# Kernel tuning notes

Measured on AMD Instinct MI355X. Metric: run time of the kernel, lower is better.

## Reference

```python
import jax, jax.numpy as jnp
import numpy as np

B, H, W, D, K = 64, 32, 32, 64, 512


def setup_inputs() -> dict:
    key = jax.random.key(0)
    k1, k2 = jax.random.split(key)
    x = jax.random.normal(k1, (B, H, W, D), dtype=jnp.float32)
    # tf.random_uniform_initializer default: U(-0.05, 0.05)
    embeddings = jax.random.uniform(k2, (D, K), dtype=jnp.float32,
                                    minval=-0.05, maxval=0.05)
    return {"x": x, "embeddings": embeddings}


def reference(x, embeddings):
    # embeddings: [D, K] (columns are codebook vectors)
    d = embeddings.shape[0]
    flat = x.reshape(-1, d)  # [N, D]
    # squared L2 distance to each code: ||z||^2 + ||e||^2 - 2 z.e
    distances = (jnp.sum(flat * flat, axis=1, keepdims=True)
                 + jnp.sum(embeddings * embeddings, axis=0)
                 - 2.0 * flat @ embeddings)  # [N, K]
    encoding_indices = jnp.argmin(distances, axis=1)  # [N]
    # one-hot @ embeddings^T  ==  gather of codebook rows
    quantized = jnp.take(embeddings.T, encoding_indices, axis=0).reshape(x.shape)
    sg = jax.lax.stop_gradient
    commitment_loss = jnp.mean((sg(quantized) - x) ** 2)  # commitment_cost = 1
    codebook_loss = jnp.mean((quantized - sg(x)) ** 2)
    loss = commitment_loss + codebook_loss
    out = x + sg(quantized - x)  # straight-through estimator
    return out, loss
```

## Files before the change

### kernel.cpp

```cpp
#include <hip/hip_runtime.h>

#define NVEC 65536
#define DIM 64
#define KCODES 512
#define VPB 128
#define NBLK 512
#define NTILE 32
#define ELS 2048.0f
#define GAP_THR 2e-4f

typedef _Float16 f16x8 __attribute__((ext_vector_type(8)));
typedef float    f32x4 __attribute__((ext_vector_type(4)));
typedef unsigned long long u64;

#define WS_EN   4
#define WS_EH   1024
#define WS_EL   (1024 + 16384)
#define WS_PART 33792
#define WS_EMBT 34816

__global__ __launch_bounds__(512, 1) void prep_kernel(const float* __restrict__ emb,
                                                      float* __restrict__ ws) {
    const int tid = threadIdx.x;
    const int b   = blockIdx.x;
    if (b == 0) {
        float s = 0.f;
#pragma unroll
        for (int d = 0; d < DIM; ++d) { float v = emb[d * KCODES + tid]; s = fmaf(v, v, s); }
        ws[WS_EN + tid] = s;
    } else if (b <= 8) {
        const int fl = (b - 1) * 512 + tid;
        const int ct = fl >> 7, s5 = (fl >> 6) & 1, l = fl & 63;
        const int k  = ct * 16 + (l & 15);
        const int d0 = s5 * 32 + (l >> 4) * 8;
        f16x8 eh, el;
#pragma unroll
        for (int e = 0; e < 8; ++e) {
            float v = emb[(d0 + e) * KCODES + k];
            _Float16 h = (_Float16)v;
            eh[e] = h;
            el[e] = (_Float16)((v - (float)h) * ELS);
        }
        ((f16x8*)(ws + WS_EH))[fl] = eh;
        ((f16x8*)(ws + WS_EL))[fl] = el;
    } else {
        __shared__ float tl[64][65];
        const int kt = b - 9;
        const int r  = tid >> 3;
        const int g  = tid & 7;
#pragma unroll
        for (int i = 0; i < 8; ++i)
            tl[r][g * 8 + i] = emb[r * KCODES + kt * 64 + g * 8 + i];
        __syncthreads();
#pragma unroll
        for (int i = 0; i < 8; ++i)
            ws[WS_EMBT + (kt * 64 + r) * 64 + g * 8 + i] = tl[g * 8 + i][r];
    }
}

__global__ __launch_bounds__(512, 2) void vq_kernel(const float* __restrict__ x,
                                                    const float* __restrict__ emb,
                                                    const float* __restrict__ ws_ro,
                                                    float* __restrict__ out,
                                                    float* __restrict__ part) {
    __shared__ f16x8 zhS[VPB][8];
    __shared__ f16x8 zlS[VPB][8];
    __shared__ float enS[KCODES];
    __shared__ float znS[VPB];
    __shared__ int   cand[VPB][2];
    __shared__ float sdf[VPB][2];
    __shared__ float exd[VPB][2];
    __shared__ int   bksel[VPB];
    __shared__ float swl[8];

    const int tid  = threadIdx.x;
    const int wid  = tid >> 6;
    const int lane = tid & 63;
    const size_t xbase = (size_t)blockIdx.x * VPB * DIM;

    enS[tid] = ws_ro[WS_EN + tid];

    {
        const int v  = tid >> 2;
        const int d0 = (tid & 3) * 16;
        const float* xp = x + xbase + v * DIM + d0;
        float4 a = *(const float4*)(xp);
        float4 b = *(const float4*)(xp + 4);
        float4 c = *(const float4*)(xp + 8);
        float4 e = *(const float4*)(xp + 12);
        float t0[8] = {a.x, a.y, a.z, a.w, b.x, b.y, b.z, b.w};
        float t1[8] = {c.x, c.y, c.z, c.w, e.x, e.y, e.z, e.w};
        float pz = 0.f;
#pragma unroll
        for (int i = 0; i < 8; ++i) pz = fmaf(t0[i], t0[i], pz);
#pragma unroll
        for (int i = 0; i < 8; ++i) pz = fmaf(t1[i], t1[i], pz);
        pz += __shfl_xor(pz, 1);
        pz += __shfl_xor(pz, 2);
        if ((tid & 3) == 0) znS[v] = pz;
        f16x8 h0, l0, h1, l1;
#pragma unroll
        for (int i = 0; i < 8; ++i) {
            _Float16 h = (_Float16)t0[i]; h0[i] = h; l0[i] = (_Float16)((t0[i] - (float)h) * ELS);
            _Float16 g = (_Float16)t1[i]; h1[i] = g; l1[i] = (_Float16)((t1[i] - (float)g) * ELS);
        }
        const int u0 = ((d0 >> 3))     ^ (v & 7);
        const int u1 = ((d0 >> 3) + 1) ^ (v & 7);
        zhS[v][u0] = h0; zhS[v][u1] = h1;
        zlS[v][u0] = l0; zlS[v][u1] = l1;
    }
    __syncthreads();

    const int vb = wid * 16;
    const int vA = vb + (lane & 15);
    const int g4 = lane >> 4;
    const int sw = vA & 7;
    f16x8 ah0 = zhS[vA][(g4)     ^ sw];
    f16x8 ah1 = zhS[vA][(4 + g4) ^ sw];
    f16x8 al0 = zlS[vA][(g4)     ^ sw];
    f16x8 al1 = zlS[vA][(4 + g4) ^ sw];
    const float zn0 = znS[vb + g4 * 4 + 0];
    const float zn1 = znS[vb + g4 * 4 + 1];
    const float zn2 = znS[vb + g4 * 4 + 2];
    const float zn3 = znS[vb + g4 * 4 + 3];

    const f16x8* ehp = (const f16x8*)(ws_ro + WS_EH);
    const f16x8* elp = (const f16x8*)(ws_ro + WS_EL);

    u64 p1_0 = ~0ull, p1_1 = ~0ull, p1_2 = ~0ull, p1_3 = ~0ull;
    u64 p2_0 = ~0ull, p2_1 = ~0ull, p2_2 = ~0ull, p2_3 = ~0ull;

    f16x8 cbh0 = ehp[lane], cbh1 = ehp[64 + lane];
    f16x8 cbl0 = elp[lane], cbl1 = elp[64 + lane];

#pragma unroll 1
    for (int ct = 0; ct < NTILE; ++ct) {
        f16x8 nbh0, nbh1, nbl0, nbl1;
        if (ct < NTILE - 1) {
            nbh0 = ehp[(ct * 2 + 2) * 64 + lane];
            nbh1 = ehp[(ct * 2 + 3) * 64 + lane];
            nbl0 = elp[(ct * 2 + 2) * 64 + lane];
            nbl1 = elp[(ct * 2 + 3) * 64 + lane];
        }
        f32x4 acch = {0.f, 0.f, 0.f, 0.f};
        f32x4 accm = {0.f, 0.f, 0.f, 0.f};
        acch = __builtin_amdgcn_mfma_f32_16x16x32_f16(ah0, cbh0, acch, 0, 0, 0);
        acch = __builtin_amdgcn_mfma_f32_16x16x32_f16(ah1, cbh1, acch, 0, 0, 0);
        accm = __builtin_amdgcn_mfma_f32_16x16x32_f16(al0, cbh0, accm, 0, 0, 0);
        accm = __builtin_amdgcn_mfma_f32_16x16x32_f16(al1, cbh1, accm, 0, 0, 0);
        accm = __builtin_amdgcn_mfma_f32_16x16x32_f16(ah0, cbl0, accm, 0, 0, 0);
        accm = __builtin_amdgcn_mfma_f32_16x16x32_f16(ah1, cbl1, accm, 0, 0, 0);
        const int   kk  = ct * 16 + (lane & 15);
        const float enk = enS[kk];
#define UPD(J, PJ1, PJ2, ZNJ) { \
        float dot  = acch[J] + accm[J] * (1.0f / ELS); \
        float dist = fmaf(-2.0f, dot, ZNJ + enk); \
        u64 p  = ((u64)__float_as_uint(dist) << 32) | (unsigned)kk; \
        u64 mx = p > PJ1 ? p : PJ1; \
        PJ1 = p < PJ1 ? p : PJ1; \
        PJ2 = mx < PJ2 ? mx : PJ2; }
        UPD(0, p1_0, p2_0, zn0) UPD(1, p1_1, p2_1, zn1)
        UPD(2, p1_2, p2_2, zn2) UPD(3, p1_3, p2_3, zn3)
#undef UPD
        if (ct < NTILE - 1) { cbh0 = nbh0; cbh1 = nbh1; cbl0 = nbl0; cbl1 = nbl1; }
    }

#pragma unroll
    for (int m = 1; m <= 8; m <<= 1) {
#define RED(PJ1, PJ2) { \
        u64 q1 = __shfl_xor(PJ1, m); u64 q2 = __shfl_xor(PJ2, m); \
        u64 lo = PJ1 < q1 ? PJ1 : q1; u64 hi = PJ1 < q1 ? q1 : PJ1; \
        u64 s2 = PJ2 < q2 ? PJ2 : q2; \
        PJ1 = lo; PJ2 = hi < s2 ? hi : s2; }
        RED(p1_0, p2_0) RED(p1_1, p2_1) RED(p1_2, p2_2) RED(p1_3, p2_3)
#undef RED
    }
    {
        const int j = lane & 15;
        if (j < 4) {
            u64 s1 = j == 0 ? p1_0 : j == 1 ? p1_1 : j == 2 ? p1_2 : p1_3;
            u64 s2 = j == 0 ? p2_0 : j == 1 ? p2_1 : j == 2 ? p2_2 : p2_3;
            const int v = vb + g4 * 4 + j;
            cand[v][0] = (int)(unsigned)s1;
            cand[v][1] = (int)(unsigned)s2;
            sdf[v][0]  = __uint_as_float((unsigned)(s1 >> 32));
            sdf[v][1]  = __uint_as_float((unsigned)(s2 >> 32));
        }
    }
    __syncthreads();

    if (tid < 256) {
        const int v = tid >> 1, c = tid & 1;
        const float dA = sdf[v][0], dB = sdf[v][1];
        float res = sdf[v][c];
        if (dB - dA <= GAP_THR) {
            const int k = cand[v][c];
            const float* xr = x + xbase + v * DIM;
            const float* er = ws_ro + WS_EMBT + k * 64;
            float zn = 0.f, dot = 0.f;
#pragma unroll
            for (int d = 0; d < DIM; ++d) {
                float xv = xr[d];
                zn  = fmaf(xv, xv, zn);
                dot = fmaf(xv, er[d], dot);
            }
            res = fmaf(-2.0f, dot, zn + enS[k]);
        }
        exd[v][c] = res;
    }
    __syncthreads();
    if (tid < VPB) {
        const int k0 = cand[tid][0], k1 = cand[tid][1];
        const float d0 = exd[tid][0], d1 = exd[tid][1];
        const bool take2 = (d1 < d0) || (d1 == d0 && k1 < k0);
        bksel[tid] = take2 ? k1 : k0;
    }
    __syncthreads();

    const int v16 = tid >> 2;
    const int j16 = (tid & 3) * 16;
    const int bk  = bksel[v16];
    const int gvec = blockIdx.x * VPB + v16;
    const float*  xg  = x + (size_t)gvec * DIM + j16;
    float*        og  = out + (size_t)gvec * DIM + j16;
    const float4* et4 = (const float4*)(ws_ro + WS_EMBT + bk * 64);

    float lossLocal = 0.f;
#pragma unroll
    for (int c = 0; c < 4; ++c) {
        float4 q  = et4[(tid & 3) * 4 + c];
        *(float4*)(og + c * 4) = q;
        float4 xa = *(const float4*)(xg + c * 4);
        float a;
        a = q.x - xa.x; lossLocal = fmaf(a, a, lossLocal);
        a = q.y - xa.y; lossLocal = fmaf(a, a, lossLocal);
        a = q.z - xa.z; lossLocal = fmaf(a, a, lossLocal);
        a = q.w - xa.w; lossLocal = fmaf(a, a, lossLocal);
    }

#pragma unroll
    for (int off = 32; off; off >>= 1) lossLocal += __shfl_down(lossLocal, off, 64);
    if (lane == 0) swl[wid] = lossLocal;
    __syncthreads();
    if (tid == 0) {
        float s = 0.f;
#pragma unroll
        for (int i = 0; i < 8; ++i) s += swl[i];
        part[WS_PART + blockIdx.x] = s;
    }
}

__global__ __launch_bounds__(256, 1) void finish_kernel(const float* __restrict__ part,
                                                        float* __restrict__ out) {
    __shared__ float sw[4];
    const int tid = threadIdx.x, lane = tid & 63, wid = tid >> 6;
    float s = part[WS_PART + tid] + part[WS_PART + tid + 256];
#pragma unroll
    for (int off = 32; off; off >>= 1) s += __shfl_down(s, off, 64);
    if (lane == 0) sw[wid] = s;
    __syncthreads();
    if (tid == 0) {
        float total = sw[0] + sw[1] + sw[2] + sw[3];
        out[(size_t)NVEC * DIM] = 2.0f * total / (float)((size_t)NVEC * DIM);
    }
}

extern "C" void kernel_launch(void* const* d_in, const int* in_sizes, int n_in,
                              void* d_out, int out_size, void* d_ws, size_t ws_size,
                              hipStream_t stream) {
    const float* x   = (const float*)d_in[0];
    const float* emb = (const float*)d_in[1];
    float* out = (float*)d_out;
    float* ws  = (float*)d_ws;

    prep_kernel<<<dim3(17), dim3(512), 0, stream>>>(emb, ws);
    vq_kernel<<<dim3(NBLK), dim3(512), 0, stream>>>(x, emb, ws, out, ws);
    finish_kernel<<<dim3(1), dim3(256), 0, stream>>>(ws, out);
}
```

Baseline: 45.73 us.

## Stage codebook chunks through double-buffered LDS and use float/int top-2 tracking

Before, every wave loaded codebook fragments from global memory on its own. Now the whole block cooperatively loads 512-entry chunks of the split-fp16 codebook into a double-buffered LDS staging area that reuses the z-fragment shared memory. The ||z||^2 term is dropped from the scan distance because it is constant per row, and packed 64-bit top-2 compares are replaced by separate float and int tracking with explicit tie-breaks. This cuts redundant global and L2 traffic per wave, at the cost of two block-wide barriers per chunk and extra LDS reads per tile.

```diff
diff --git a/kernel.cpp b/kernel.cpp
--- a/kernel.cpp
+++ b/kernel.cpp
@@ -5,13 +5,12 @@
 #define KCODES 512
 #define VPB 128
 #define NBLK 512
-#define NTILE 32
 #define ELS 2048.0f
+#define INV_ELS (1.0f / 2048.0f)
 #define GAP_THR 2e-4f
 
 typedef _Float16 f16x8 __attribute__((ext_vector_type(8)));
 typedef float    f32x4 __attribute__((ext_vector_type(4)));
-typedef unsigned long long u64;
 
 #define WS_EN   4
 #define WS_EH   1024
@@ -59,14 +58,14 @@
 }
 
 __global__ __launch_bounds__(512, 2) void vq_kernel(const float* __restrict__ x,
-                                                    const float* __restrict__ emb,
                                                     const float* __restrict__ ws_ro,
                                                     float* __restrict__ out,
                                                     float* __restrict__ part) {
-    __shared__ f16x8 zhS[VPB][8];
-    __shared__ f16x8 zlS[VPB][8];
+    __shared__ alignas(16) unsigned char ovlRaw[32768];
+    f16x8 (*zhS)[8] = reinterpret_cast<f16x8(*)[8]>(ovlRaw);
+    f16x8 (*zlS)[8] = reinterpret_cast<f16x8(*)[8]>(ovlRaw + 16384);
+    f16x8* stgS     = reinterpret_cast<f16x8*>(ovlRaw);
     __shared__ float enS[KCODES];
-    __shared__ float znS[VPB];
     __shared__ int   cand[VPB][2];
     __shared__ float sdf[VPB][2];
     __shared__ float exd[VPB][2];
@@ -77,6 +76,12 @@
     const int wid  = tid >> 6;
     const int lane = tid & 63;
     const size_t xbase = (size_t)blockIdx.x * VPB * DIM;
+
+    const f16x8* ehp = (const f16x8*)(ws_ro + WS_EH);
+    const f16x8* elp = (const f16x8*)(ws_ro + WS_EL);
+
+    f16x8 pgh = ehp[tid];
+    f16x8 pgl = elp[tid];
 
     enS[tid] = ws_ro[WS_EN + tid];
 
@@ -90,14 +95,6 @@
         float4 e = *(const float4*)(xp + 12);
         float t0[8] = {a.x, a.y, a.z, a.w, b.x, b.y, b.z, b.w};
         float t1[8] = {c.x, c.y, c.z, c.w, e.x, e.y, e.z, e.w};
-        float pz = 0.f;
-#pragma unroll
-        for (int i = 0; i < 8; ++i) pz = fmaf(t0[i], t0[i], pz);
-#pragma unroll
-        for (int i = 0; i < 8; ++i) pz = fmaf(t1[i], t1[i], pz);
-        pz += __shfl_xor(pz, 1);
-        pz += __shfl_xor(pz, 2);
-        if ((tid & 3) == 0) znS[v] = pz;
         f16x8 h0, l0, h1, l1;
 #pragma unroll
         for (int i = 0; i < 8; ++i) {
@@ -119,82 +116,103 @@
     f16x8 ah1 = zhS[vA][(4 + g4) ^ sw];
     f16x8 al0 = zlS[vA][(g4)     ^ sw];
     f16x8 al1 = zlS[vA][(4 + g4) ^ sw];
-    const float zn0 = znS[vb + g4 * 4 + 0];
-    const float zn1 = znS[vb + g4 * 4 + 1];
-    const float zn2 = znS[vb + g4 * 4 + 2];
-    const float zn3 = znS[vb + g4 * 4 + 3];
-
-    const f16x8* ehp = (const f16x8*)(ws_ro + WS_EH);
-    const f16x8* elp = (const f16x8*)(ws_ro + WS_EL);
-
-    u64 p1_0 = ~0ull, p1_1 = ~0ull, p1_2 = ~0ull, p1_3 = ~0ull;
-    u64 p2_0 = ~0ull, p2_1 = ~0ull, p2_2 = ~0ull, p2_3 = ~0ull;
-
-    f16x8 cbh0 = ehp[lane], cbh1 = ehp[64 + lane];
-    f16x8 cbl0 = elp[lane], cbl1 = elp[64 + lane];
+    __syncthreads();
+
+    stgS[tid]       = pgh;
+    stgS[512 + tid] = pgl;
+    __syncthreads();
+
+    float best[4]  = {3.4e38f, 3.4e38f, 3.4e38f, 3.4e38f};
+    float best2[4] = {3.4e38f, 3.4e38f, 3.4e38f, 3.4e38f};
+    int   bk1[4]   = {0, 0, 0, 0};
+    int   bk2[4]   = {0, 0, 0, 0};
 
 #pragma unroll 1
-    for (int ct = 0; ct < NTILE; ++ct) {
-        f16x8 nbh0, nbh1, nbl0, nbl1;
-        if (ct < NTILE - 1) {
-            nbh0 = ehp[(ct * 2 + 2) * 64 + lane];
-            nbh1 = ehp[(ct * 2 + 3) * 64 + lane];
-            nbl0 = elp[(ct * 2 + 2) * 64 + lane];
-            nbl1 = elp[(ct * 2 + 3) * 64 + lane];
-        }
-        f32x4 acch = {0.f, 0.f, 0.f, 0.f};
-        f32x4 accm = {0.f, 0.f, 0.f, 0.f};
-        acch = __builtin_amdgcn_mfma_f32_16x16x32_f16(ah0, cbh0, acch, 0, 0, 0);
-        acch = __builtin_amdgcn_mfma_f32_16x16x32_f16(ah1, cbh1, acch, 0, 0, 0);
-        accm = __builtin_amdgcn_mfma_f32_16x16x32_f16(al0, cbh0, accm, 0, 0, 0);
-        accm = __builtin_amdgcn_mfma_f32_16x16x32_f16(al1, cbh1, accm, 0, 0, 0);
-        accm = __builtin_amdgcn_mfma_f32_16x16x32_f16(ah0, cbl0, accm, 0, 0, 0);
-        accm = __builtin_amdgcn_mfma_f32_16x16x32_f16(ah1, cbl1, accm, 0, 0, 0);
-        const int   kk  = ct * 16 + (lane & 15);
-        const float enk = enS[kk];
-#define UPD(J, PJ1, PJ2, ZNJ) { \
-        float dot  = acch[J] + accm[J] * (1.0f / ELS); \
-        float dist = fmaf(-2.0f, dot, ZNJ + enk); \
-        u64 p  = ((u64)__float_as_uint(dist) << 32) | (unsigned)kk; \
-        u64 mx = p > PJ1 ? p : PJ1; \
-        PJ1 = p < PJ1 ? p : PJ1; \
-        PJ2 = mx < PJ2 ? mx : PJ2; }
-        UPD(0, p1_0, p2_0, zn0) UPD(1, p1_1, p2_1, zn1)
-        UPD(2, p1_2, p2_2, zn2) UPD(3, p1_3, p2_3, zn3)
-#undef UPD
-        if (ct < NTILE - 1) { cbh0 = nbh0; cbh1 = nbh1; cbl0 = nbl0; cbl1 = nbl1; }
+    for (int c = 0; c < 8; ++c) {
+        const int buf = (c & 1) * 1024;
+        f16x8 ngh, ngl;
+        if (c < 7) {
+            ngh = ehp[(c + 1) * 512 + tid];
+            ngl = elp[(c + 1) * 512 + tid];
+        }
+#pragma unroll
+        for (int lt = 0; lt < 4; ++lt) {
+            const int ct = c * 4 + lt;
+            f16x8 bh0 = stgS[buf + (2 * lt)     * 64 + lane];
+            f16x8 bh1 = stgS[buf + (2 * lt + 1) * 64 + lane];
+            f16x8 bl0 = stgS[buf + 512 + (2 * lt)     * 64 + lane];
+            f16x8 bl1 = stgS[buf + 512 + (2 * lt + 1) * 64 + lane];
+            f32x4 acch = {0.f, 0.f, 0.f, 0.f};
+            f32x4 accm = {0.f, 0.f, 0.f, 0.f};
+            acch = __builtin_amdgcn_mfma_f32_16x16x32_f16(ah0, bh0, acch, 0, 0, 0);
+            acch = __builtin_amdgcn_mfma_f32_16x16x32_f16(ah1, bh1, acch, 0, 0, 0);
+            accm = __builtin_amdgcn_mfma_f32_16x16x32_f16(al0, bh0, accm, 0, 0, 0);
+            accm = __builtin_amdgcn_mfma_f32_16x16x32_f16(al1, bh1, accm, 0, 0, 0);
+            accm = __builtin_amdgcn_mfma_f32_16x16x32_f16(ah0, bl0, accm, 0, 0, 0);
+            accm = __builtin_amdgcn_mfma_f32_16x16x32_f16(ah1, bl1, accm, 0, 0, 0);
+            const int   kk  = ct * 16 + (lane & 15);
+            const float enk = enS[kk];
+#pragma unroll
+            for (int j = 0; j < 4; ++j) {
+                float dot = fmaf(accm[j], INV_ELS, acch[j]);
+                float sc  = fmaf(-2.0f, dot, enk);
+                bool  c1  = sc < best[j];
+                bool  c2  = sc < best2[j];
+                bk2[j]    = c1 ? bk1[j] : (c2 ? kk : bk2[j]);
+                best2[j]  = fminf(best2[j], fmaxf(sc, best[j]));
+                bk1[j]    = c1 ? kk : bk1[j];
+                best[j]   = fminf(sc, best[j]);
+            }
+        }
+        __syncthreads();
+        if (c < 7) {
+            const int nbuf = ((c + 1) & 1) * 1024;
+            stgS[nbuf + tid]       = ngh;
+            stgS[nbuf + 512 + tid] = ngl;
+        }
+        __syncthreads();
     }
 
 #pragma unroll
     for (int m = 1; m <= 8; m <<= 1) {
-#define RED(PJ1, PJ2) { \
-        u64 q1 = __shfl_xor(PJ1, m); u64 q2 = __shfl_xor(PJ2, m); \
-        u64 lo = PJ1 < q1 ? PJ1 : q1; u64 hi = PJ1 < q1 ? q1 : PJ1; \
-        u64 s2 = PJ2 < q2 ? PJ2 : q2; \
-        PJ1 = lo; PJ2 = hi < s2 ? hi : s2; }
-        RED(p1_0, p2_0) RED(p1_1, p2_1) RED(p1_2, p2_2) RED(p1_3, p2_3)
-#undef RED
+#pragma unroll
+        for (int j = 0; j < 4; ++j) {
+            float qb  = __shfl_xor(best[j],  m);
+            int   qk  = __shfl_xor(bk1[j],   m);
+            float q2  = __shfl_xor(best2[j], m);
+            int   qk2 = __shfl_xor(bk2[j],   m);
+            bool  t1  = (qb < best[j]) || (qb == best[j] && qk < bk1[j]);
+            float lb  = t1 ? best[j] : qb;
+            int   lk  = t1 ? bk1[j]  : qk;
+            float nb  = t1 ? qb : best[j];
+            int   nk  = t1 ? qk : bk1[j];
+            bool  ta  = (best2[j] < q2) || (best2[j] == q2 && bk2[j] < qk2);
+            float sb  = ta ? best2[j] : q2;
+            int   sk  = ta ? bk2[j]   : qk2;
+            bool  tb  = (lb < sb) || (lb == sb && lk < sk);
+            best2[j]  = tb ? lb : sb;
+            bk2[j]    = tb ? lk : sk;
+            best[j]   = nb;
+            bk1[j]    = nk;
+        }
     }
     {
         const int j = lane & 15;
         if (j < 4) {
-            u64 s1 = j == 0 ? p1_0 : j == 1 ? p1_1 : j == 2 ? p1_2 : p1_3;
-            u64 s2 = j == 0 ? p2_0 : j == 1 ? p2_1 : j == 2 ? p2_2 : p2_3;
             const int v = vb + g4 * 4 + j;
-            cand[v][0] = (int)(unsigned)s1;
-            cand[v][1] = (int)(unsigned)s2;
-            sdf[v][0]  = __uint_as_float((unsigned)(s1 >> 32));
-            sdf[v][1]  = __uint_as_float((unsigned)(s2 >> 32));
+            cand[v][0] = bk1[j];
+            cand[v][1] = bk2[j];
+            sdf[v][0]  = best[j];
+            sdf[v][1]  = best2[j];
         }
     }
     __syncthreads();
 
     if (tid < 256) {
-        const int v = tid >> 1, c = tid & 1;
-        const float dA = sdf[v][0], dB = sdf[v][1];
-        float res = sdf[v][c];
-        if (dB - dA <= GAP_THR) {
-            const int k = cand[v][c];
+        const int v = tid >> 1, cc = tid & 1;
+        float res = sdf[v][cc];
+        if (sdf[v][1] - sdf[v][0] <= GAP_THR) {
+            const int k = cand[v][cc];
             const float* xr = x + xbase + v * DIM;
             const float* er = ws_ro + WS_EMBT + k * 64;
             float zn = 0.f, dot = 0.f;
@@ -206,7 +224,7 @@
             }
             res = fmaf(-2.0f, dot, zn + enS[k]);
         }
-        exd[v][c] = res;
+        exd[v][cc] = res;
     }
     __syncthreads();
     if (tid < VPB) {
@@ -274,6 +292,6 @@
     float* ws  = (float*)d_ws;
 
     prep_kernel<<<dim3(17), dim3(512), 0, stream>>>(emb, ws);
-    vq_kernel<<<dim3(NBLK), dim3(512), 0, stream>>>(x, emb, ws, out, ws);
+    vq_kernel<<<dim3(NBLK), dim3(512), 0, stream>>>(x, ws, out, ws);
     finish_kernel<<<dim3(1), dim3(256), 0, stream>>>(ws, out);
 }
```

Result: slower. 51.41 us (+12.4%).
